# Optimization experiments

Hardware: AMD Instinct MI355X
Metric: run time of the kernel (lower is better)

Reference implementation:

```python
import jax, jax.numpy as jnp
import numpy as np

L, D, S, K, V, R, E, C = 256, 300, 16, 16, 100000, 6, 2048, 7
SW = 1            # slide_win; window = 2*SW+1 = 3
LAMB = 0.5
NEG = -1e9


def setup_inputs() -> dict:
    key = jax.random.key(0)
    ks = jax.random.split(key, 24)
    utt_emb = jax.random.normal(ks[0], (L, D), jnp.float32)
    str_src = jax.random.randint(ks[1], (E,), 0, L)
    str_dst = jax.random.randint(ks[2], (E,), 0, L)
    str_edge_type = jax.random.randint(ks[3], (E,), 0, R)
    src_ids = jax.random.randint(ks[4], (3, L, S), 0, V)
    src_valid = jax.random.uniform(ks[5], (3, L, S)) < 0.9
    cpt_src_ids = jnp.where(src_valid, src_ids, -1)
    dst_ids = jax.random.randint(ks[6], (3, L, S, K), 0, V)
    dst_valid = jnp.logical_and(jax.random.uniform(ks[7], (3, L, S, K)) < 0.8, src_valid[..., None])
    cpt_dst_ids = jnp.where(dst_valid, dst_ids, -1)
    cpt_weight = jax.random.uniform(ks[8], (3, L, S, K), jnp.float32)
    cpt_sentic = jax.random.normal(ks[9], (3, L, S, K), jnp.float32) * 0.5
    cpt_table = jax.random.normal(ks[10], (V, D), jnp.float32) * 0.02
    W_basis = jax.random.normal(ks[11], (2, D, D), jnp.float32) * 0.02
    comp = jax.random.normal(ks[12], (R, 2), jnp.float32)
    W_self = jax.random.normal(ks[13], (D, D), jnp.float32) * 0.02
    b_rgcn = jnp.zeros((D,), jnp.float32)
    Wq = jax.random.normal(ks[14], (D, D), jnp.float32) * 0.02
    Wk = jax.random.normal(ks[15], (D, D), jnp.float32) * 0.02
    Wv = jax.random.normal(ks[16], (D, D), jnp.float32) * 0.02
    Wo = jax.random.normal(ks[17], (D, D), jnp.float32) * 0.02
    r_vecs = jax.random.uniform(ks[18], (3, D), jnp.float32)  # isa/causes/hcontext relation vectors
    W_fuse = jax.random.normal(ks[19], (3 * D, D), jnp.float32) * 0.02
    b_fuse = jnp.zeros((D,), jnp.float32)
    W_out = jax.random.normal(ks[20], (D, C), jnp.float32) * 0.02
    b_out = jnp.zeros((C,), jnp.float32)
    return dict(utt_emb=utt_emb, str_src=str_src, str_dst=str_dst, str_edge_type=str_edge_type,
                cpt_src_ids=cpt_src_ids, cpt_dst_ids=cpt_dst_ids, cpt_weight=cpt_weight,
                cpt_sentic=cpt_sentic, cpt_table=cpt_table, W_basis=W_basis, comp=comp,
                W_self=W_self, b_rgcn=b_rgcn, Wq=Wq, Wk=Wk, Wv=Wv, Wo=Wo, r_vecs=r_vecs,
                W_fuse=W_fuse, b_fuse=b_fuse, W_out=W_out, b_out=b_out)


def reference(utt_emb, str_src, str_dst, str_edge_type, cpt_src_ids, cpt_dst_ids,
              cpt_weight, cpt_sentic, cpt_table, W_basis, comp, W_self, b_rgcn,
              Wq, Wk, Wv, Wo, r_vecs, W_fuse, b_fuse, W_out, b_out):
    H, dh, W = 2, D // 2, 2 * SW + 1
    # ---- RelGraphConv (basis decomposition, num_bases=2, sum aggregation + self-loop) ----
    W_rel = jnp.einsum('rb,bio->rio', comp, W_basis)                       # [R,D,D]
    msg = jnp.einsum('ei,eio->eo', utt_emb[str_src], W_rel[str_edge_type])  # [E,D]
    hidden_rgcn = jax.ops.segment_sum(msg, str_dst, num_segments=L) + utt_emb @ W_self + b_rgcn
    # ---- RelAtt: multi-head attention over sliding window, keep center utterance ----
    ids = jnp.concatenate([jnp.zeros((SW,), jnp.int32), jnp.arange(L, dtype=jnp.int32), jnp.full((SW,), L - 1, jnp.int32)])
    win = ids[jnp.arange(L)[:, None] + jnp.arange(W)[None, :]]             # [L,W]
    x = utt_emb[win]                                                       # [L,W,D]
    sh = lambda t: t.reshape(L, W, H, dh).transpose(0, 2, 1, 3)
    q, k, v = sh(x @ Wq), sh(x @ Wk), sh(x @ Wv)
    attn = jax.nn.softmax(jnp.einsum('lhqd,lhkd->lhqk', q, k) / jnp.sqrt(jnp.float32(dh)), axis=-1)
    relatt_out = (jnp.einsum('lhqk,lhkd->lhqd', attn, v).transpose(0, 2, 1, 3).reshape(L, W, D) @ Wo)[:, SW, :]
    # ---- symbolic reasoning over 3 relation types (padded, vectorized) ----
    src_mask = cpt_src_ids >= 0                                            # [3,L,S]
    dst_mask = cpt_dst_ids >= 0                                            # [3,L,S,K]
    src_emb = cpt_table[jnp.maximum(cpt_src_ids, 0)]                       # [3,L,S,D]
    dst_emb = cpt_table[jnp.maximum(cpt_dst_ids, 0)]                       # [3,L,S,K,D]
    u = relatt_out[None, :, None, None, :]                                 # [1,L,1,1,D]
    cos = jnp.abs(jnp.sum(u * dst_emb, -1) / (jnp.linalg.norm(relatt_out, axis=-1)[None, :, None, None] * jnp.linalg.norm(dst_emb, axis=-1) + 1e-8))
    omega = LAMB * cpt_weight * cos + (1.0 - LAMB) * jnp.abs(cpt_sentic)
    alpha1 = jax.nn.softmax(jnp.where(dst_mask, omega, NEG), axis=-1) * dst_mask  # [3,L,S,K]
    cpt = alpha1[..., None] * dst_emb                                      # [3,L,S,K,D]
    re_dot = r_vecs[:, None, None, None, :] * cpt                          # relation-weighted neighbor emb
    s = jnp.sum(src_emb[..., None, :] * re_dot, -1)                        # [3,L,S,K]
    alpha2 = jax.nn.softmax(jnp.where(dst_mask, s, NEG), axis=-1) * dst_mask
    src2 = src_emb + jnp.sum(alpha2[..., None] * re_dot, axis=3)           # [3,L,S,D]
    nodes = src2.transpose(1, 0, 2, 3).reshape(L, 3 * S, D)
    node_mask = src_mask.transpose(1, 0, 2).reshape(L, 3 * S)
    score = jnp.einsum('lnd,ld->ln', nodes, relatt_out)
    att = jax.nn.softmax(jnp.where(node_mask, score, NEG), axis=-1) * node_mask
    sym = jnp.einsum('ln,lnd->ld', att, nodes)
    sym = sym * jnp.any(node_mask, axis=-1, keepdims=True)                 # symbolic_mask
    # ---- fusion + classifier ----
    feat = jnp.concatenate([hidden_rgcn, relatt_out, sym], axis=-1)        # [L,3D]
    return jax.nn.log_softmax(jax.nn.relu(feat @ W_fuse + b_fuse) @ W_out + b_out, axis=-1)
```

## Files before the change

### kernel.cpp

```cpp
#include <hip/hip_runtime.h>
#include <math.h>

#define Lq 256
#define Dm 300
#define Sq 16
#define Kc 16
#define Eq 2048
#define D4 75

__global__ __launch_bounds__(256) void mm6_kernel(
    const float* __restrict__ utt,
    const float* __restrict__ Wb,
    const float* __restrict__ Wself,
    const float* __restrict__ brgcn,
    const float* __restrict__ Wq,
    const float* __restrict__ Wk,
    const float* __restrict__ Wv,
    float* __restrict__ P0, float* __restrict__ P1,
    float* __restrict__ Hrg, float* __restrict__ Q,
    float* __restrict__ Km, float* __restrict__ Vm)
{
    const int m = blockIdx.y;
    const float* W; float* Y; const float* bias = nullptr;
    switch (m) {
      case 0: W = Wb;          Y = P0; break;
      case 1: W = Wb + 90000;  Y = P1; break;
      case 2: W = Wself;       Y = Hrg; bias = brgcn; break;
      case 3: W = Wq;          Y = Q; break;
      case 4: W = Wk;          Y = Km; break;
      default: W = Wv;         Y = Vm; break;
    }
    const int row0 = blockIdx.x * 4;
    __shared__ float xs[4][Dm];
    for (int i = threadIdx.x; i < 4*Dm; i += 256)
        xs[i/Dm][i%Dm] = utt[(row0 + i/Dm)*Dm + (i%Dm)];
    __syncthreads();
    for (int c = threadIdx.x; c < Dm; c += 256) {
        float a0=0.f,a1=0.f,a2=0.f,a3=0.f;
        #pragma unroll 10
        for (int d = 0; d < Dm; ++d) {
            float wv = W[d*Dm + c];
            a0 += xs[0][d]*wv; a1 += xs[1][d]*wv;
            a2 += xs[2][d]*wv; a3 += xs[3][d]*wv;
        }
        float b = bias ? bias[c] : 0.f;
        Y[(row0+0)*Dm+c] = a0+b;
        Y[(row0+1)*Dm+c] = a1+b;
        Y[(row0+2)*Dm+c] = a2+b;
        Y[(row0+3)*Dm+c] = a3+b;
    }
}

__global__ __launch_bounds__(64) void rgcn_edge_kernel(
    const int* __restrict__ src, const int* __restrict__ dst, const int* __restrict__ et,
    const float* __restrict__ comp, const float* __restrict__ P0,
    const float* __restrict__ P1, float* __restrict__ Hrg)
{
    int e = blockIdx.x;
    int s = src[e], d = dst[e], r = et[e];
    float c0 = comp[r*2], c1 = comp[r*2+1];
    for (int i = threadIdx.x; i < Dm; i += 64) {
        float msg = c0*P0[s*Dm+i] + c1*P1[s*Dm+i];
        atomicAdd(&Hrg[d*Dm+i], msg);
    }
}

__global__ __launch_bounds__(256) void attn_out_kernel(
    const float* __restrict__ Q, const float* __restrict__ Kmat,
    const float* __restrict__ Vmat, const float* __restrict__ W,
    float* __restrict__ Y, float* __restrict__ nrm)
{
    const int row0 = blockIdx.x * 4;
    const int tid = threadIdx.x, lane = tid & 63, wave = tid >> 6;
    __shared__ float xs[4][Dm];
    __shared__ float s_n[4];
    if (tid < 4) s_n[tid] = 0.f;

    const int l = row0 + wave;
    const int w0 = l > 0 ? l-1 : 0;
    const int w1 = l;
    const int w2 = l < Lq-1 ? l+1 : Lq-1;
    const int win[3] = {w0, w1, w2};

    float sc[2][3];
    #pragma unroll
    for (int h = 0; h < 2; ++h) {
      #pragma unroll
      for (int w = 0; w < 3; ++w) {
        float acc = 0.f;
        const float* qp = Q + l*Dm + h*150;
        const float* kp = Kmat + win[w]*Dm + h*150;
        for (int d = lane; d < 150; d += 64) acc += qp[d]*kp[d];
        #pragma unroll
        for (int off = 32; off; off >>= 1) acc += __shfl_xor(acc, off);
        sc[h][w] = acc * 0.081649658092772603f;
      }
    }
    float attn[2][3];
    #pragma unroll
    for (int h = 0; h < 2; ++h) {
      float m = fmaxf(sc[h][0], fmaxf(sc[h][1], sc[h][2]));
      float e0 = expf(sc[h][0]-m), e1 = expf(sc[h][1]-m), e2 = expf(sc[h][2]-m);
      float iz = 1.f/(e0+e1+e2);
      attn[h][0]=e0*iz; attn[h][1]=e1*iz; attn[h][2]=e2*iz;
    }
    for (int d = lane; d < Dm; d += 64) {
      int h = d / 150;
      xs[wave][d] = attn[h][0]*Vmat[w0*Dm+d] + attn[h][1]*Vmat[w1*Dm+d]
                  + attn[h][2]*Vmat[w2*Dm+d];
    }
    __syncthreads();

    float sq0=0.f, sq1=0.f, sq2=0.f, sq3=0.f;
    for (int c = tid; c < Dm; c += 256) {
        float a0=0.f,a1=0.f,a2=0.f,a3=0.f;
        #pragma unroll 10
        for (int d = 0; d < Dm; ++d) {
            float wv = W[d*Dm + c];
            a0 += xs[0][d]*wv; a1 += xs[1][d]*wv;
            a2 += xs[2][d]*wv; a3 += xs[3][d]*wv;
        }
        Y[(row0+0)*Dm+c] = a0;
        Y[(row0+1)*Dm+c] = a1;
        Y[(row0+2)*Dm+c] = a2;
        Y[(row0+3)*Dm+c] = a3;
        sq0 += a0*a0; sq1 += a1*a1; sq2 += a2*a2; sq3 += a3*a3;
    }
    #pragma unroll
    for (int off = 32; off; off >>= 1) {
        sq0 += __shfl_down(sq0, off);
        sq1 += __shfl_down(sq1, off);
        sq2 += __shfl_down(sq2, off);
        sq3 += __shfl_down(sq3, off);
    }
    if (lane == 0) {
        atomicAdd(&s_n[0], sq0); atomicAdd(&s_n[1], sq1);
        atomicAdd(&s_n[2], sq2); atomicAdd(&s_n[3], sq3);
    }
    __syncthreads();
    if (tid < 4) nrm[row0 + tid] = sqrtf(s_n[tid]);
}

__global__ __launch_bounds__(256) void concept_kernel(
    const int* __restrict__ src_ids,
    const int* __restrict__ dst_ids,
    const float* __restrict__ cw,
    const float* __restrict__ csen,
    const float* __restrict__ table,
    const float* __restrict__ relatt,
    const float* __restrict__ unorm,
    const float* __restrict__ rvecs,
    float* __restrict__ src2,
    float* __restrict__ score)
{
    int cell = blockIdx.x;
    int g = cell / (Lq*Sq);
    int l = (cell / Sq) % Lq;
    int s = cell % Sq;
    int tid = threadIdx.x, lane = tid & 63, wave = tid >> 6;

    int sid = src_ids[cell];
    if (sid < 0) {
        if (tid == 0) score[l*48 + g*Sq + s] = -1e30f;
        return;
    }

    __shared__ float4 s_rows[Kc][D4+1];
    __shared__ float4 s_u[D4+1], s_src[D4+1], s_r[D4+1], s_w[D4+1];
    __shared__ float  s_du[Kc], s_dw[Kc], s_dn[Kc], s_beta[Kc];
    __shared__ float  s_part[16];
    __shared__ int    s_dst[Kc];

    const int base = cell * Kc;
    if (tid < D4)              s_u[tid]        = ((const float4*)(relatt + l*Dm))[tid];
    else if (tid < 2*D4)       s_src[tid-D4]   = ((const float4*)(table + (size_t)sid*Dm))[tid-D4];
    else if (tid < 3*D4)       s_r[tid-2*D4]   = ((const float4*)(rvecs + g*Dm))[tid-2*D4];
    else if (tid < 3*D4+Kc)    s_dst[tid-3*D4] = dst_ids[base + tid - 3*D4];
    __syncthreads();
    if (tid < D4) {
        float4 a = s_src[tid], b = s_r[tid];
        s_w[tid] = make_float4(a.x*b.x, a.y*b.y, a.z*b.z, a.w*b.w);
    }
    __syncthreads();

    int grp = lane >> 4, gl = lane & 15;
    int k = wave*4 + grp;
    int did = s_dst[k];
    float du = 0.f, dw = 0.f, dn = 0.f;
    if (did >= 0) {
        const float4* rp = (const float4*)(table + (size_t)did*Dm);
        #pragma unroll
        for (int j = 0; j < 5; ++j) {
            int idx = gl + 16*j;
            if (idx < D4) {
                float4 v = rp[idx];
                s_rows[k][idx] = v;
                float4 u = s_u[idx], w = s_w[idx];
                du += v.x*u.x + v.y*u.y + v.z*u.z + v.w*u.w;
                dw += v.x*w.x + v.y*w.y + v.z*w.z + v.w*w.w;
                dn += v.x*v.x + v.y*v.y + v.z*v.z + v.w*v.w;
            }
        }
    }
    #pragma unroll
    for (int off = 8; off; off >>= 1) {
        du += __shfl_down(du, off, 16);
        dw += __shfl_down(dw, off, 16);
        dn += __shfl_down(dn, off, 16);
    }
    if (gl == 0) { s_du[k] = du; s_dw[k] = dw; s_dn[k] = dn; }
    __syncthreads();

    if (wave == 0 && lane < Kc) {
        int kk = lane;
        int msk = (s_dst[kk] >= 0) ? 1 : 0;
        float pre = -1e30f;
        if (msk) {
            float cosv = fabsf(s_du[kk]) / (unorm[l]*sqrtf(s_dn[kk]) + 1e-8f);
            pre = 0.5f*cw[base+kk]*cosv + 0.5f*fabsf(csen[base+kk]);
        }
        float mx = pre;
        #pragma unroll
        for (int off = 8; off; off >>= 1) mx = fmaxf(mx, __shfl_xor(mx, off, 16));
        float e1 = msk ? expf(pre - mx) : 0.f;
        float Z = e1;
        #pragma unroll
        for (int off = 8; off; off >>= 1) Z += __shfl_xor(Z, off, 16);
        float beta = 0.f;
        if (Z > 0.f) {
            float a1 = e1 / Z;
            float sv = msk ? a1 * s_dw[kk] : -1e30f;
            float mx2 = sv;
            #pragma unroll
            for (int off = 8; off; off >>= 1) mx2 = fmaxf(mx2, __shfl_xor(mx2, off, 16));
            float e2 = msk ? expf(sv - mx2) : 0.f;
            float Z2 = e2;
            #pragma unroll
            for (int off = 8; off; off >>= 1) Z2 += __shfl_xor(Z2, off, 16);
            beta = a1 * (e2 / Z2);
        }
        s_beta[kk] = beta;
    }
    __syncthreads();

    float dot = 0.f;
    if (tid < D4) {
        float4 acc = make_float4(0.f, 0.f, 0.f, 0.f);
        #pragma unroll
        for (int kk = 0; kk < Kc; ++kk) {
            float b = s_beta[kk];
            if (b != 0.f) {
                float4 v = s_rows[kk][tid];
                acc.x += b*v.x; acc.y += b*v.y; acc.z += b*v.z; acc.w += b*v.w;
            }
        }
        float4 sv = s_src[tid], rv = s_r[tid];
        float4 o;
        o.x = sv.x + rv.x*acc.x;
        o.y = sv.y + rv.y*acc.y;
        o.z = sv.z + rv.z*acc.z;
        o.w = sv.w + rv.w*acc.w;
        ((float4*)(src2 + (size_t)cell*Dm))[tid] = o;
        float4 u = s_u[tid];
        dot = o.x*u.x + o.y*u.y + o.z*u.z + o.w*u.w;
    }
    if (wave == 1 && lane < 16) s_part[lane] = dot;
    __syncthreads();
    if (wave == 0) {
        float v = dot + (lane < 16 ? s_part[lane] : 0.f);
        #pragma unroll
        for (int off = 32; off; off >>= 1) v += __shfl_down(v, off);
        if (lane == 0)
            score[l*48 + g*Sq + s] = v;
    }
}

__global__ __launch_bounds__(256) void fuse1_kernel(
    const float* __restrict__ Hrg, const float* __restrict__ relatt,
    const float* __restrict__ score, const float* __restrict__ src2,
    const float* __restrict__ Wf, float* __restrict__ part)
{
    int l = blockIdx.x, j = blockIdx.y, tid = threadIdx.x;
    const int k0 = j * 100;
    const int seg = j / 3;
    const int koff = (j % 3) * 100;
    __shared__ float s_f[100];
    __shared__ float s_att[48];
    if (seg == 2 && tid < 64) {
        float sv = (tid < 48) ? score[l*48+tid] : -1e30f;
        float mx = sv;
        #pragma unroll
        for (int off = 32; off; off >>= 1) mx = fmaxf(mx, __shfl_xor(mx, off));
        float e = (sv > -1e29f) ? expf(sv-mx) : 0.f;
        float Z = e;
        #pragma unroll
        for (int off = 32; off; off >>= 1) Z += __shfl_xor(Z, off);
        float iZ = (Z > 0.f) ? 1.f/Z : 0.f;
        if (tid < 48) s_att[tid] = e*iZ;
    }
    __syncthreads();
    if (tid < 100) {
        if (seg == 0)      s_f[tid] = Hrg[l*Dm + koff + tid];
        else if (seg == 1) s_f[tid] = relatt[l*Dm + koff + tid];
        else {
            float acc = 0.f;
            for (int n = 0; n < 48; ++n) {
                float a = s_att[n];
                if (a != 0.f) {
                    int gg = n >> 4, ss = n & 15;
                    acc += a * src2[(size_t)((gg*Lq + l)*Sq + ss)*Dm + koff + tid];
                }
            }
            s_f[tid] = acc;
        }
    }
    __syncthreads();
    for (int c = tid; c < Dm; c += 256) {
        float acc = 0.f;
        #pragma unroll 10
        for (int i = 0; i < 100; ++i)
            acc += s_f[i] * Wf[(k0 + i)*Dm + c];
        part[(size_t)j*Lq*Dm + l*Dm + c] = acc;
    }
}

__global__ __launch_bounds__(256) void fuse2_kernel(
    const float* __restrict__ part, const float* __restrict__ bf,
    const float* __restrict__ Wout, const float* __restrict__ bout,
    float* __restrict__ out)
{
    int l = blockIdx.x, tid = threadIdx.x;
    __shared__ float s_h1[Dm];
    __shared__ float s_logit[7];
    for (int c = tid; c < Dm; c += 256) {
        float acc = bf[c];
        #pragma unroll
        for (int j = 0; j < 9; ++j)
            acc += part[(size_t)j*Lq*Dm + l*Dm + c];
        s_h1[c] = fmaxf(acc, 0.f);
    }
    __syncthreads();
    if (tid < 64) {
        for (int c = 0; c < 7; ++c) {
            float acc = 0.f;
            for (int i = tid; i < Dm; i += 64) acc += s_h1[i]*Wout[i*7+c];
            for (int off = 32; off > 0; off >>= 1) acc += __shfl_down(acc, off);
            if (tid == 0) s_logit[c] = acc + bout[c];
        }
    }
    __syncthreads();
    if (tid == 0) {
        float mx = s_logit[0];
        for (int c = 1; c < 7; ++c) mx = fmaxf(mx, s_logit[c]);
        float Z = 0.f;
        for (int c = 0; c < 7; ++c) Z += expf(s_logit[c]-mx);
        float lz = logf(Z) + mx;
        for (int c = 0; c < 7; ++c) out[l*7+c] = s_logit[c] - lz;
    }
}

extern "C" void kernel_launch(void* const* d_in, const int* in_sizes, int n_in,
                              void* d_out, int out_size, void* d_ws, size_t ws_size,
                              hipStream_t stream)
{
    const float* utt   = (const float*)d_in[0];
    const int* str_src = (const int*)d_in[1];
    const int* str_dst = (const int*)d_in[2];
    const int* str_et  = (const int*)d_in[3];
    const int* csrc    = (const int*)d_in[4];
    const int* cdst    = (const int*)d_in[5];
    const float* cw    = (const float*)d_in[6];
    const float* csen  = (const float*)d_in[7];
    const float* table = (const float*)d_in[8];
    const float* Wb    = (const float*)d_in[9];
    const float* comp  = (const float*)d_in[10];
    const float* Wself = (const float*)d_in[11];
    const float* brg   = (const float*)d_in[12];
    const float* Wq    = (const float*)d_in[13];
    const float* Wk    = (const float*)d_in[14];
    const float* Wv    = (const float*)d_in[15];
    const float* Wo    = (const float*)d_in[16];
    const float* rvec  = (const float*)d_in[17];
    const float* Wf    = (const float*)d_in[18];
    const float* bf    = (const float*)d_in[19];
    const float* Wout  = (const float*)d_in[20];
    const float* bout  = (const float*)d_in[21];

    float* ws   = (float*)d_ws;
    float* P0   = ws;
    float* P1   = P0 + 76800;
    float* Q    = P1 + 76800;
    float* Km   = Q  + 76800;
    float* Vm   = Km + 76800;
    float* Hrg  = Vm + 76800;
    float* rel  = Hrg + 76800;
    float* unrm = rel + 76800;
    float* score= unrm + 256;
    float* part = score + 12288;
    float* src2 = part + 691200;

    mm6_kernel<<<dim3(64,6), 256, 0, stream>>>(utt, Wb, Wself, brg, Wq, Wk, Wv,
                                               P0, P1, Hrg, Q, Km, Vm);
    rgcn_edge_kernel<<<Eq, 64, 0, stream>>>(str_src, str_dst, str_et, comp, P0, P1, Hrg);
    attn_out_kernel<<<64, 256, 0, stream>>>(Q, Km, Vm, Wo, rel, unrm);
    concept_kernel<<<3*Lq*Sq, 256, 0, stream>>>(csrc, cdst, cw, csen, table, rel,
                                                unrm, rvec, src2, score);
    fuse1_kernel<<<dim3(Lq,9), 256, 0, stream>>>(Hrg, rel, score, src2, Wf, part);
    fuse2_kernel<<<Lq, 256, 0, stream>>>(part, bf, Wout, bout, (float*)d_out);
}
```

Baseline: 369.2 us.

## Split attention output per row and keep concept rows in registers

The attention-output kernel now launches one block per row and column half (512 blocks instead of 64). This trades the reuse of each Wo load across four rows for more parallelism. The per-row norm is no longer written by that kernel; each concept block recomputes it from the relatt row instead. The concept kernel also keeps the gathered neighbour rows in registers rather than a large shared array, and reduces the beta-weighted sum with shuffles plus a small per-wave shared buffer. This cuts shared memory use and may allow more blocks per CU.

Result: slower. 378.4 us (+2.5%).

```diff
diff --git a/kernel.cpp b/kernel.cpp
--- a/kernel.cpp
+++ b/kernel.cpp
@@ -68,77 +68,55 @@
 __global__ __launch_bounds__(256) void attn_out_kernel(
     const float* __restrict__ Q, const float* __restrict__ Kmat,
     const float* __restrict__ Vmat, const float* __restrict__ W,
-    float* __restrict__ Y, float* __restrict__ nrm)
-{
-    const int row0 = blockIdx.x * 4;
+    float* __restrict__ Y)
+{
+    const int l = blockIdx.x, half = blockIdx.y;
     const int tid = threadIdx.x, lane = tid & 63, wave = tid >> 6;
-    __shared__ float xs[4][Dm];
-    __shared__ float s_n[4];
-    if (tid < 4) s_n[tid] = 0.f;
-
-    const int l = row0 + wave;
-    const int w0 = l > 0 ? l-1 : 0;
-    const int w1 = l;
-    const int w2 = l < Lq-1 ? l+1 : Lq-1;
-    const int win[3] = {w0, w1, w2};
-
-    float sc[2][3];
-    #pragma unroll
-    for (int h = 0; h < 2; ++h) {
-      #pragma unroll
-      for (int w = 0; w < 3; ++w) {
+    __shared__ float xs[Dm];
+
+    if (wave == 0) {
+        const int w0 = l > 0 ? l-1 : 0;
+        const int w1 = l;
+        const int w2 = l < Lq-1 ? l+1 : Lq-1;
+        const int win[3] = {w0, w1, w2};
+        float sc[2][3];
+        #pragma unroll
+        for (int h = 0; h < 2; ++h) {
+          #pragma unroll
+          for (int w = 0; w < 3; ++w) {
+            float acc = 0.f;
+            const float* qp = Q + l*Dm + h*150;
+            const float* kp = Kmat + win[w]*Dm + h*150;
+            for (int d = lane; d < 150; d += 64) acc += qp[d]*kp[d];
+            #pragma unroll
+            for (int off = 32; off; off >>= 1) acc += __shfl_xor(acc, off);
+            sc[h][w] = acc * 0.081649658092772603f;
+          }
+        }
+        float attn[2][3];
+        #pragma unroll
+        for (int h = 0; h < 2; ++h) {
+          float m = fmaxf(sc[h][0], fmaxf(sc[h][1], sc[h][2]));
+          float e0 = expf(sc[h][0]-m), e1 = expf(sc[h][1]-m), e2 = expf(sc[h][2]-m);
+          float iz = 1.f/(e0+e1+e2);
+          attn[h][0]=e0*iz; attn[h][1]=e1*iz; attn[h][2]=e2*iz;
+        }
+        for (int d = lane; d < Dm; d += 64) {
+          int h = d / 150;
+          xs[d] = attn[h][0]*Vmat[w0*Dm+d] + attn[h][1]*Vmat[w1*Dm+d]
+                + attn[h][2]*Vmat[w2*Dm+d];
+        }
+    }
+    __syncthreads();
+
+    if (tid < 150) {
+        const int c = half*150 + tid;
         float acc = 0.f;
-        const float* qp = Q + l*Dm + h*150;
-        const float* kp = Kmat + win[w]*Dm + h*150;
-        for (int d = lane; d < 150; d += 64) acc += qp[d]*kp[d];
-        #pragma unroll
-        for (int off = 32; off; off >>= 1) acc += __shfl_xor(acc, off);
-        sc[h][w] = acc * 0.081649658092772603f;
-      }
-    }
-    float attn[2][3];
-    #pragma unroll
-    for (int h = 0; h < 2; ++h) {
-      float m = fmaxf(sc[h][0], fmaxf(sc[h][1], sc[h][2]));
-      float e0 = expf(sc[h][0]-m), e1 = expf(sc[h][1]-m), e2 = expf(sc[h][2]-m);
-      float iz = 1.f/(e0+e1+e2);
-      attn[h][0]=e0*iz; attn[h][1]=e1*iz; attn[h][2]=e2*iz;
-    }
-    for (int d = lane; d < Dm; d += 64) {
-      int h = d / 150;
-      xs[wave][d] = attn[h][0]*Vmat[w0*Dm+d] + attn[h][1]*Vmat[w1*Dm+d]
-                  + attn[h][2]*Vmat[w2*Dm+d];
-    }
-    __syncthreads();
-
-    float sq0=0.f, sq1=0.f, sq2=0.f, sq3=0.f;
-    for (int c = tid; c < Dm; c += 256) {
-        float a0=0.f,a1=0.f,a2=0.f,a3=0.f;
         #pragma unroll 10
-        for (int d = 0; d < Dm; ++d) {
-            float wv = W[d*Dm + c];
-            a0 += xs[0][d]*wv; a1 += xs[1][d]*wv;
-            a2 += xs[2][d]*wv; a3 += xs[3][d]*wv;
-        }
-        Y[(row0+0)*Dm+c] = a0;
-        Y[(row0+1)*Dm+c] = a1;
-        Y[(row0+2)*Dm+c] = a2;
-        Y[(row0+3)*Dm+c] = a3;
-        sq0 += a0*a0; sq1 += a1*a1; sq2 += a2*a2; sq3 += a3*a3;
-    }
-    #pragma unroll
-    for (int off = 32; off; off >>= 1) {
-        sq0 += __shfl_down(sq0, off);
-        sq1 += __shfl_down(sq1, off);
-        sq2 += __shfl_down(sq2, off);
-        sq3 += __shfl_down(sq3, off);
-    }
-    if (lane == 0) {
-        atomicAdd(&s_n[0], sq0); atomicAdd(&s_n[1], sq1);
-        atomicAdd(&s_n[2], sq2); atomicAdd(&s_n[3], sq3);
-    }
-    __syncthreads();
-    if (tid < 4) nrm[row0 + tid] = sqrtf(s_n[tid]);
+        for (int d = 0; d < Dm; ++d)
+            acc += xs[d] * W[d*Dm + c];
+        Y[l*Dm + c] = acc;
+    }
 }
 
 __global__ __launch_bounds__(256) void concept_kernel(
@@ -148,7 +126,6 @@
     const float* __restrict__ csen,
     const float* __restrict__ table,
     const float* __restrict__ relatt,
-    const float* __restrict__ unorm,
     const float* __restrict__ rvecs,
     float* __restrict__ src2,
     float* __restrict__ score)
@@ -165,10 +142,10 @@
         return;
     }
 
-    __shared__ float4 s_rows[Kc][D4+1];
-    __shared__ float4 s_u[D4+1], s_src[D4+1], s_r[D4+1], s_w[D4+1];
+    __shared__ float4 s_u[D4+1], s_src[D4+1], s_r[D4+1];
+    __shared__ float4 s_part[4][D4+1];
     __shared__ float  s_du[Kc], s_dw[Kc], s_dn[Kc], s_beta[Kc];
-    __shared__ float  s_part[16];
+    __shared__ float  s_sc[16];
     __shared__ int    s_dst[Kc];
 
     const int base = cell * Kc;
@@ -177,28 +154,35 @@
     else if (tid < 3*D4)       s_r[tid-2*D4]   = ((const float4*)(rvecs + g*Dm))[tid-2*D4];
     else if (tid < 3*D4+Kc)    s_dst[tid-3*D4] = dst_ids[base + tid - 3*D4];
     __syncthreads();
-    if (tid < D4) {
-        float4 a = s_src[tid], b = s_r[tid];
-        s_w[tid] = make_float4(a.x*b.x, a.y*b.y, a.z*b.z, a.w*b.w);
-    }
-    __syncthreads();
+
+    float un = 0.f;
+    for (int idx = lane; idx < D4; idx += 64) {
+        float4 u = s_u[idx];
+        un += u.x*u.x + u.y*u.y + u.z*u.z + u.w*u.w;
+    }
+    #pragma unroll
+    for (int off = 32; off; off >>= 1) un += __shfl_xor(un, off);
+    float unorm_l = sqrtf(un);
 
     int grp = lane >> 4, gl = lane & 15;
     int k = wave*4 + grp;
     int did = s_dst[k];
+    float4 v[5];
     float du = 0.f, dw = 0.f, dn = 0.f;
+    #pragma unroll
+    for (int j = 0; j < 5; ++j) v[j] = make_float4(0.f,0.f,0.f,0.f);
     if (did >= 0) {
         const float4* rp = (const float4*)(table + (size_t)did*Dm);
         #pragma unroll
         for (int j = 0; j < 5; ++j) {
             int idx = gl + 16*j;
             if (idx < D4) {
-                float4 v = rp[idx];
-                s_rows[k][idx] = v;
-                float4 u = s_u[idx], w = s_w[idx];
-                du += v.x*u.x + v.y*u.y + v.z*u.z + v.w*u.w;
-                dw += v.x*w.x + v.y*w.y + v.z*w.z + v.w*w.w;
-                dn += v.x*v.x + v.y*v.y + v.z*v.z + v.w*v.w;
+                float4 t = rp[idx];
+                v[j] = t;
+                float4 u = s_u[idx], sr = s_src[idx], rr = s_r[idx];
+                du += t.x*u.x + t.y*u.y + t.z*u.z + t.w*u.w;
+                dw += t.x*sr.x*rr.x + t.y*sr.y*rr.y + t.z*sr.z*rr.z + t.w*sr.w*rr.w;
+                dn += t.x*t.x + t.y*t.y + t.z*t.z + t.w*t.w;
             }
         }
     }
@@ -216,7 +200,7 @@
         int msk = (s_dst[kk] >= 0) ? 1 : 0;
         float pre = -1e30f;
         if (msk) {
-            float cosv = fabsf(s_du[kk]) / (unorm[l]*sqrtf(s_dn[kk]) + 1e-8f);
+            float cosv = fabsf(s_du[kk]) / (unorm_l*sqrtf(s_dn[kk]) + 1e-8f);
             pre = 0.5f*cw[base+kk]*cosv + 0.5f*fabsf(csen[base+kk]);
         }
         float mx = pre;
@@ -243,17 +227,33 @@
     }
     __syncthreads();
 
+    float b = s_beta[k];
+    #pragma unroll
+    for (int j = 0; j < 5; ++j) {
+        v[j].x *= b; v[j].y *= b; v[j].z *= b; v[j].w *= b;
+        v[j].x += __shfl_xor(v[j].x, 16); v[j].x += __shfl_xor(v[j].x, 32);
+        v[j].y += __shfl_xor(v[j].y, 16); v[j].y += __shfl_xor(v[j].y, 32);
+        v[j].z += __shfl_xor(v[j].z, 16); v[j].z += __shfl_xor(v[j].z, 32);
+        v[j].w += __shfl_xor(v[j].w, 16); v[j].w += __shfl_xor(v[j].w, 32);
+    }
+    if (grp == 0) {
+        #pragma unroll
+        for (int j = 0; j < 5; ++j) {
+            int idx = gl + 16*j;
+            if (idx < D4) s_part[wave][idx] = v[j];
+        }
+    }
+    __syncthreads();
+
     float dot = 0.f;
     if (tid < D4) {
-        float4 acc = make_float4(0.f, 0.f, 0.f, 0.f);
-        #pragma unroll
-        for (int kk = 0; kk < Kc; ++kk) {
-            float b = s_beta[kk];
-            if (b != 0.f) {
-                float4 v = s_rows[kk][tid];
-                acc.x += b*v.x; acc.y += b*v.y; acc.z += b*v.z; acc.w += b*v.w;
-            }
-        }
+        float4 p0 = s_part[0][tid], p1 = s_part[1][tid];
+        float4 p2 = s_part[2][tid], p3 = s_part[3][tid];
+        float4 acc;
+        acc.x = p0.x+p1.x+p2.x+p3.x;
+        acc.y = p0.y+p1.y+p2.y+p3.y;
+        acc.z = p0.z+p1.z+p2.z+p3.z;
+        acc.w = p0.w+p1.w+p2.w+p3.w;
         float4 sv = s_src[tid], rv = s_r[tid];
         float4 o;
         o.x = sv.x + rv.x*acc.x;
@@ -264,14 +264,14 @@
         float4 u = s_u[tid];
         dot = o.x*u.x + o.y*u.y + o.z*u.z + o.w*u.w;
     }
-    if (wave == 1 && lane < 16) s_part[lane] = dot;
+    if (wave == 1 && lane < 16) s_sc[lane] = dot;
     __syncthreads();
     if (wave == 0) {
-        float v = dot + (lane < 16 ? s_part[lane] : 0.f);
-        #pragma unroll
-        for (int off = 32; off; off >>= 1) v += __shfl_down(v, off);
+        float vv = dot + (lane < 16 ? s_sc[lane] : 0.f);
+        #pragma unroll
+        for (int off = 32; off; off >>= 1) vv += __shfl_down(vv, off);
         if (lane == 0)
-            score[l*48 + g*Sq + s] = v;
+            score[l*48 + g*Sq + s] = vv;
     }
 }
 
@@ -394,17 +394,16 @@
     float* Vm   = Km + 76800;
     float* Hrg  = Vm + 76800;
     float* rel  = Hrg + 76800;
-    float* unrm = rel + 76800;
-    float* score= unrm + 256;
+    float* score= rel + 76800;
     float* part = score + 12288;
     float* src2 = part + 691200;
 
     mm6_kernel<<<dim3(64,6), 256, 0, stream>>>(utt, Wb, Wself, brg, Wq, Wk, Wv,
                                                P0, P1, Hrg, Q, Km, Vm);
     rgcn_edge_kernel<<<Eq, 64, 0, stream>>>(str_src, str_dst, str_et, comp, P0, P1, Hrg);
-    attn_out_kernel<<<64, 256, 0, stream>>>(Q, Km, Vm, Wo, rel, unrm);
+    attn_out_kernel<<<dim3(Lq,2), 256, 0, stream>>>(Q, Km, Vm, Wo, rel);
     concept_kernel<<<3*Lq*Sq, 256, 0, stream>>>(csrc, cdst, cw, csen, table, rel,
-                                                unrm, rvec, src2, score);
+                                                rvec, src2, score);
     fuse1_kernel<<<dim3(Lq,9), 256, 0, stream>>>(Hrg, rel, score, src2, Wf, part);
     fuse2_kernel<<<Lq, 256, 0, stream>>>(part, bf, Wout, bout, (float*)d_out);
 }
```
